# Performance work log

Measured on AMD Instinct MI355X. Metric: run time of the kernel, lower is better.

Reference implementation:

```python
import jax, jax.numpy as jnp
import numpy as np

DIM = 1536
NH = 12
HD = DIM // NH  # 128
F_, H_, W_ = 16, 16, 16
L = F_ * H_ * W_  # 4096


def _precompute_freqs(dim, max_positions, base=10000.0):
    # [max_positions, dim//2] angles
    half = dim // 2
    inv = 1.0 / base ** (np.arange(0, half * 2, 2, dtype=np.float32) / (half * 2))
    pos = np.arange(max_positions, dtype=np.float32)
    return pos[:, None] * inv[None, :]


def _get_3d_freqs(head_dim, F, H, W, base=10000.0):
    half_hd = head_dim // 2
    n_t = max(1, head_dim // 4 // 2)
    n_h = max(1, head_dim * 3 // 8 // 2)
    n_w = half_hd - n_t - n_h
    ft = _precompute_freqs(n_t * 2, F, base)  # [F, n_t]
    fh = _precompute_freqs(n_h * 2, H, base)  # [H, n_h]
    fw = _precompute_freqs(n_w * 2, W, base)  # [W, n_w]
    f_idx = np.broadcast_to(ft[:, None, None, :], (F, H, W, n_t))
    h_idx = np.broadcast_to(fh[None, :, None, :], (F, H, W, n_h))
    w_idx = np.broadcast_to(fw[None, None, :, :], (F, H, W, n_w))
    return np.concatenate([f_idx, h_idx, w_idx], axis=-1).reshape(F * H * W, half_hd)


def setup_inputs() -> dict:
    key = jax.random.key(0)
    ks = jax.random.split(key, 9)
    s = 1.0 / np.sqrt(DIM)
    x = jax.random.normal(ks[0], (1, L, DIM), dtype=jnp.float32)
    freqs = jnp.asarray(_get_3d_freqs(HD, F_, H_, W_), dtype=jnp.float32)
    Wq = jax.random.normal(ks[1], (DIM, DIM), dtype=jnp.float32) * s
    bq = jax.random.normal(ks[2], (DIM,), dtype=jnp.float32) * 0.01
    Wk = jax.random.normal(ks[3], (DIM, DIM), dtype=jnp.float32) * s
    bk = jax.random.normal(ks[4], (DIM,), dtype=jnp.float32) * 0.01
    Wv = jax.random.normal(ks[5], (DIM, DIM), dtype=jnp.float32) * s
    bv = jax.random.normal(ks[6], (DIM,), dtype=jnp.float32) * 0.01
    Wo = jax.random.normal(ks[7], (DIM, DIM), dtype=jnp.float32) * s
    bo = jax.random.normal(ks[8], (DIM,), dtype=jnp.float32) * 0.01
    return {"x": x, "freqs": freqs, "Wq": Wq, "bq": bq, "Wk": Wk, "bk": bk,
            "Wv": Wv, "bv": bv, "Wo": Wo, "bo": bo}


def _apply_rotary(t, cos_v, sin_v):
    # t: [B, Nh, L, Hd]; cos_v/sin_v: [L, Hd//2]
    B, Nh, Lq, Hd = t.shape
    t2 = t.reshape(B, Nh, Lq, Hd // 2, 2)
    x0, x1 = t2[..., 0], t2[..., 1]
    r0 = x0 * cos_v - x1 * sin_v
    r1 = x0 * sin_v + x1 * cos_v
    return jnp.stack([r0, r1], axis=-1).reshape(B, Nh, Lq, Hd)


def reference(x, freqs, Wq, bq, Wk, bk, Wv, bv, Wo, bo):
    B, Lq, D = x.shape
    Nh, Hd = NH, D // NH
    q = (x @ Wq + bq).reshape(B, Lq, Nh, Hd).transpose(0, 2, 1, 3)
    k = (x @ Wk + bk).reshape(B, Lq, Nh, Hd).transpose(0, 2, 1, 3)
    v = (x @ Wv + bv).reshape(B, Lq, Nh, Hd).transpose(0, 2, 1, 3)
    cos_v = jnp.cos(freqs)  # [L, Hd//2]
    sin_v = jnp.sin(freqs)
    q = _apply_rotary(q, cos_v, sin_v)
    k = _apply_rotary(k, cos_v, sin_v)
    scale = 1.0 / jnp.sqrt(jnp.asarray(Hd, dtype=x.dtype))
    scores = jnp.einsum('bhqd,bhkd->bhqk', q, k) * scale
    attn = jax.nn.softmax(scores, axis=-1)
    out = jnp.einsum('bhqk,bhkd->bhqd', attn, v)
    out = out.transpose(0, 2, 1, 3).reshape(B, Lq, D)
    return out @ Wo + bo
```

## Files before the change

### kernel.cpp

```cpp
#include <hip/hip_runtime.h>

#define DIM 1536
#define NH  12
#define HD  128
#define SEQ 4096

typedef unsigned short u16;
typedef unsigned int   u32;
typedef __attribute__((ext_vector_type(8))) short bf16x8;
typedef __attribute__((ext_vector_type(4))) float f32x4;

static __device__ __forceinline__ u16 f2bf(float f) {
    u32 u = __float_as_uint(f);
    u32 r = u + 0x7FFFu + ((u >> 16) & 1u);
    return (u16)(r >> 16);
}
static __device__ __forceinline__ float bf2f(u16 h) {
    return __uint_as_float(((u32)h) << 16);
}
static __device__ __forceinline__ u32 pack2(float a, float b) {
    return (u32)f2bf(a) | ((u32)f2bf(b) << 16);
}

#define GLL(g, s) __builtin_amdgcn_global_load_lds( \
    (const __attribute__((address_space(1))) void*)(g), \
    (__attribute__((address_space(3))) void*)(s), 16, 0, 0)

__global__ __launch_bounds__(256) void k_cvt_x(const float* __restrict__ x, u16* __restrict__ xb) {
    int gid = blockIdx.x * 256 + threadIdx.x;
    const float4* p = (const float4*)x + (size_t)gid * 2;
    float4 a = p[0], b = p[1];
    uint4 o;
    o.x = pack2(a.x, a.y); o.y = pack2(a.z, a.w);
    o.z = pack2(b.x, b.y); o.w = pack2(b.z, b.w);
    *(uint4*)(xb + (size_t)gid * 8) = o;
}

__global__ __launch_bounds__(256) void k_transpose_w(const float* __restrict__ Wq, const float* __restrict__ Wk,
                                                     const float* __restrict__ Wv, const float* __restrict__ Wo,
                                                     u16* __restrict__ wqkv, u16* __restrict__ wot) {
    __shared__ float tile[32][33];
    int z = blockIdx.z;
    const float* W = z == 0 ? Wq : z == 1 ? Wk : z == 2 ? Wv : Wo;
    u16* out = z < 3 ? (wqkv + (size_t)z * DIM * DIM) : wot;
    int tx = threadIdx.x, ty = threadIdx.y;
    int c0 = blockIdx.x * 32, r0 = blockIdx.y * 32;
#pragma unroll
    for (int i = 0; i < 4; i++)
        tile[ty + i * 8][tx] = W[(size_t)(r0 + ty + i * 8) * DIM + c0 + tx];
    __syncthreads();
#pragma unroll
    for (int i = 0; i < 4; i++)
        out[(size_t)(c0 + ty + i * 8) * DIM + r0 + tx] = f2bf(tile[tx][ty + i * 8]);
}

__global__ __launch_bounds__(256) void k_tr_v(const u16* __restrict__ vb, u16* __restrict__ vt) {
    __shared__ u16 tile[32][33];
    int h = blockIdx.z;
    int l0 = blockIdx.x * 32, d0 = blockIdx.y * 32;
    int tx = threadIdx.x, ty = threadIdx.y;
    const u16* src = vb + (size_t)h * SEQ * HD;
    u16* dst = vt + (size_t)h * HD * SEQ;
#pragma unroll
    for (int i = 0; i < 4; i++)
        tile[ty + i * 8][tx] = src[(size_t)(l0 + ty + i * 8) * HD + d0 + tx];
    __syncthreads();
#pragma unroll
    for (int i = 0; i < 4; i++)
        dst[(size_t)(d0 + ty + i * 8) * SEQ + l0 + tx] = tile[tx][ty + i * 8];
}

__global__ __launch_bounds__(256) void k_prep(const float* __restrict__ fr, const float* __restrict__ bq,
                                              const float* __restrict__ bk, const float* __restrict__ bv,
                                              float2* __restrict__ cs, float* __restrict__ bqkv) {
    int gid = blockIdx.x * 256 + threadIdx.x;
    float f = fr[gid];
    cs[gid] = make_float2(cosf(f), sinf(f));
    if (gid < 3 * DIM)
        bqkv[gid] = gid < DIM ? bq[gid] : gid < 2 * DIM ? bk[gid - DIM] : bv[gid - 2 * DIM];
}

__global__ __launch_bounds__(256) void k_gemm(const u16* __restrict__ A, const u16* __restrict__ B,
                                              const float* __restrict__ bias, int Kdim, int mode,
                                              u16* __restrict__ qo, u16* __restrict__ ko,
                                              u16* __restrict__ vo, float* __restrict__ outf) {
    __shared__ u16 As[128 * 32];
    __shared__ u16 Bs[128 * 32];
    const int tid = threadIdx.x;
    const int w = tid >> 6, l = tid & 63;
    const int wr = w >> 1, wc = w & 1;
    const int lr = l & 15, lg = l >> 4;
    const int m0 = blockIdx.y * 128, n0 = blockIdx.x * 128;
    f32x4 acc[4][4] = {};

    const int srow = l >> 2;
    const int scol = (((l & 3) * 16) ^ (((l >> 2) & 3) << 4)) >> 1;

    for (int kt = 0; kt < Kdim; kt += 32) {
        __syncthreads();
#pragma unroll
        for (int c2 = 0; c2 < 2; ++c2) {
            int c = w * 2 + c2;
            int row = c * 16 + srow;
            GLL(A + (size_t)(m0 + row) * Kdim + kt + scol, As + c * 512);
            GLL(B + (size_t)(n0 + row) * Kdim + kt + scol, Bs + c * 512);
        }
        __syncthreads();
        bf16x8 af[4], bg[4];
#pragma unroll
        for (int i = 0; i < 4; i++) {
            int co = (lg * 8) ^ ((lr & 3) << 3);
            af[i] = *(const bf16x8*)(As + (wr * 64 + i * 16 + lr) * 32 + co);
            bg[i] = *(const bf16x8*)(Bs + (wc * 64 + i * 16 + lr) * 32 + co);
        }
#pragma unroll
        for (int i = 0; i < 4; i++)
#pragma unroll
            for (int j = 0; j < 4; j++)
                acc[i][j] = __builtin_amdgcn_mfma_f32_16x16x32_bf16(af[i], bg[j], acc[i][j], 0, 0, 0);
    }

#pragma unroll
    for (int j = 0; j < 4; j++) {
        int gc = n0 + wc * 64 + j * 16 + lr;
        float bb = bias[gc];
#pragma unroll
        for (int i = 0; i < 4; i++) {
            int gr0 = m0 + wr * 64 + i * 16 + lg * 4;
            if (mode == 0) {
                int t = gc / DIM;
                int rr = gc % DIM;
                int hh = rr >> 7, hd = rr & 127;
                u16* dst = t == 0 ? qo : t == 1 ? ko : vo;
                size_t base = (size_t)hh * SEQ * HD + hd;
#pragma unroll
                for (int r = 0; r < 4; r++)
                    dst[base + (size_t)(gr0 + r) * HD] = f2bf(acc[i][j][r] + bb);
            } else {
#pragma unroll
                for (int r = 0; r < 4; r++)
                    outf[(size_t)(gr0 + r) * DIM + gc] = acc[i][j][r] + bb;
            }
        }
    }
}

__global__ __launch_bounds__(256) void k_rope(u16* __restrict__ qb, u16* __restrict__ kb,
                                              const float2* __restrict__ cs) {
    int gid = blockIdx.x * 256 + threadIdx.x;
    const int T = NH * SEQ * 64;
    u16* buf = gid < T ? qb : kb;
    int r = gid < T ? gid : gid - T;
    int hh = r / (SEQ * 64);
    int rr = r % (SEQ * 64);
    int ll = rr >> 6, ii = rr & 63;
    size_t off = ((size_t)hh * SEQ + ll) * HD + 2 * ii;
    u32 pk = *(const u32*)(buf + off);
    float x0 = bf2f((u16)(pk & 0xFFFFu)), x1 = bf2f((u16)(pk >> 16));
    float2 c = cs[ll * 64 + ii];
    float r0 = x0 * c.x - x1 * c.y;
    float r1 = x0 * c.y + x1 * c.x;
    *(u32*)(buf + off) = pack2(r0, r1);
}

__global__ __launch_bounds__(256, 3) void k_attn(const u16* __restrict__ qb, const u16* __restrict__ kbuf,
                                                 const u16* __restrict__ vt, u16* __restrict__ attnb) {
    __shared__ u16 Ks[64 * 128];
    __shared__ u16 Vs[128 * 64];
    __shared__ u32 Pl[4 * 16 * 36];
    const int tid = threadIdx.x;
    const int w = tid >> 6, l = tid & 63;
    const int lr = l & 15, lg = l >> 4;
    int bid = blockIdx.x;
    int gw = (bid & 7) * 96 + (bid >> 3);
    const int h = gw >> 6;
    const int q0 = (gw & 63) << 6;
    const size_t hb = (size_t)h * SEQ * HD;
    constexpr float SCL2 = 0.08838834764831845f * 1.4426950408889634f;
    constexpr float THR = 5.0f;

    bf16x8 qf[4];
    {
        int qrow = q0 + w * 16 + lr;
#pragma unroll
        for (int c = 0; c < 4; c++)
            qf[c] = *(const bf16x8*)(qb + hb + (size_t)qrow * HD + c * 32 + lg * 8);
    }
    f32x4 O[8] = {};
    float m_run = -1e30f, lsum = 0.f;
    u32* Plw = Pl + w * 576 + lr * 36;

    for (int kt = 0; kt < SEQ; kt += 64) {
        __syncthreads();
#pragma unroll
        for (int c = 0; c < 4; c++) {
            int cc = w * 4 + c;
            int key = cc * 4 + lg;
            int d0 = ((lr * 16) ^ ((key & 7) << 4)) >> 1;
            GLL(kbuf + hb + (size_t)(kt + key) * HD + d0, Ks + cc * 512);
            int dd = cc * 8 + (l >> 3);
            int c0 = (((l & 7) * 16) ^ ((l >> 3) << 4)) >> 1;
            GLL(vt + hb + (size_t)dd * SEQ + kt + c0, Vs + cc * 512);
        }
        __syncthreads();

        f32x4 ST[4];
#pragma unroll
        for (int jb = 0; jb < 4; jb++) {
            f32x4 st = {};
            int row = jb * 16 + lr;
            int rx = (row & 7) << 4;
#pragma unroll
            for (int c = 0; c < 4; c++) {
                int cb = ((c * 64 + lg * 16) ^ rx) >> 1;
                bf16x8 kf = *(const bf16x8*)(Ks + row * 128 + cb);
                st = __builtin_amdgcn_mfma_f32_16x16x32_bf16(kf, qf[c], st, 0, 0, 0);
            }
            ST[jb] = st;
        }

        float mx = ST[0][0];
#pragma unroll
        for (int jb = 0; jb < 4; jb++)
#pragma unroll
            for (int r = 0; r < 4; r++)
                mx = fmaxf(mx, ST[jb][r]);
        mx = fmaxf(mx, __shfl_xor(mx, 16));
        mx = fmaxf(mx, __shfl_xor(mx, 32));
        float mt = mx * SCL2;
        bool grow = mt > m_run + THR;
        float m_new = grow ? mt : m_run;
        if (__any(grow)) {
            float alpha = grow ? __builtin_amdgcn_exp2f(m_run - m_new) : 1.0f;
            lsum *= alpha;
            m_run = m_new;
            float aO[4];
#pragma unroll
            for (int r = 0; r < 4; r++)
                aO[r] = __shfl(alpha, lg * 4 + r);
#pragma unroll
            for (int f = 0; f < 8; f++)
#pragma unroll
                for (int r = 0; r < 4; r++)
                    O[f][r] *= aO[r];
        }
        float ps = 0.f;
#pragma unroll
        for (int jb = 0; jb < 4; jb++)
#pragma unroll
            for (int r = 0; r < 4; r++) {
                float p = __builtin_amdgcn_exp2f(fmaf(ST[jb][r], SCL2, -m_new));
                ST[jb][r] = p;
                ps += p;
            }
        lsum += ps;

#pragma unroll
        for (int jb = 0; jb < 4; jb++) {
            u32 p0, p1;
            asm("v_cvt_pk_bf16_f32 %0, %1, %2" : "=v"(p0) : "v"(ST[jb][0]), "v"(ST[jb][1]));
            asm("v_cvt_pk_bf16_f32 %0, %1, %2" : "=v"(p1) : "v"(ST[jb][2]), "v"(ST[jb][3]));
            Plw[jb * 8 + lg * 2 + 0] = p0;
            Plw[jb * 8 + lg * 2 + 1] = p1;
        }
        bf16x8 pa0 = *(const bf16x8*)(Plw + lg * 4);
        bf16x8 pa1 = *(const bf16x8*)(Plw + 16 + lg * 4);

#pragma unroll
        for (int f = 0; f < 8; f++) {
            int vrow = f * 16 + lr;
            int rx = (vrow & 7) << 4;
            bf16x8 v0 = *(const bf16x8*)(Vs + vrow * 64 + (((lg * 16) ^ rx) >> 1));
            O[f] = __builtin_amdgcn_mfma_f32_16x16x32_bf16(pa0, v0, O[f], 0, 0, 0);
            bf16x8 v1 = *(const bf16x8*)(Vs + vrow * 64 + (((64 + lg * 16) ^ rx) >> 1));
            O[f] = __builtin_amdgcn_mfma_f32_16x16x32_bf16(pa1, v1, O[f], 0, 0, 0);
        }
    }

    lsum += __shfl_xor(lsum, 16);
    lsum += __shfl_xor(lsum, 32);
    float li[4];
#pragma unroll
    for (int r = 0; r < 4; r++)
        li[r] = 1.0f / __shfl(lsum, lg * 4 + r);
#pragma unroll
    for (int f = 0; f < 8; f++) {
        int col = h * HD + f * 16 + lr;
#pragma unroll
        for (int r = 0; r < 4; r++) {
            int row = q0 + w * 16 + lg * 4 + r;
            attnb[(size_t)row * DIM + col] = f2bf(O[f][r] * li[r]);
        }
    }
}

extern "C" void kernel_launch(void* const* d_in, const int* in_sizes, int n_in,
                              void* d_out, int out_size, void* d_ws, size_t ws_size,
                              hipStream_t stream) {
    (void)in_sizes; (void)n_in; (void)out_size; (void)ws_size;
    const float* x  = (const float*)d_in[0];
    const float* fr = (const float*)d_in[1];
    const float* Wq = (const float*)d_in[2];
    const float* bq = (const float*)d_in[3];
    const float* Wk = (const float*)d_in[4];
    const float* bk = (const float*)d_in[5];
    const float* Wv = (const float*)d_in[6];
    const float* bv = (const float*)d_in[7];
    const float* Wo = (const float*)d_in[8];
    const float* bo = (const float*)d_in[9];
    float* out = (float*)d_out;

    char* ws = (char*)d_ws;
    size_t off = 0;
    auto alloc = [&](size_t b) { char* p = ws + off; off = (off + b + 255) & ~(size_t)255; return p; };
    u16*   xb    = (u16*)alloc((size_t)SEQ * DIM * 2);
    u16*   wqkv  = (u16*)alloc((size_t)3 * DIM * DIM * 2);
    u16*   wot   = (u16*)alloc((size_t)DIM * DIM * 2);
    float* bqkv  = (float*)alloc((size_t)3 * DIM * 4);
    u16*   qb    = (u16*)alloc((size_t)SEQ * DIM * 2);
    u16*   kb    = (u16*)alloc((size_t)SEQ * DIM * 2);
    u16*   vb    = (u16*)alloc((size_t)SEQ * DIM * 2);
    u16*   vtb   = (u16*)alloc((size_t)SEQ * DIM * 2);
    u16*   attnb = (u16*)alloc((size_t)SEQ * DIM * 2);
    float2* cs   = (float2*)alloc((size_t)SEQ * 64 * 8);

    k_cvt_x<<<3072, 256, 0, stream>>>(x, xb);
    k_transpose_w<<<dim3(48, 48, 4), dim3(32, 8), 0, stream>>>(Wq, Wk, Wv, Wo, wqkv, wot);
    k_prep<<<1024, 256, 0, stream>>>(fr, bq, bk, bv, cs, bqkv);
    k_gemm<<<dim3(36, 32), 256, 0, stream>>>(xb, wqkv, bqkv, DIM, 0, qb, kb, vb, nullptr);
    k_rope<<<24576, 256, 0, stream>>>(qb, kb, cs);
    k_tr_v<<<dim3(128, 4, 12), dim3(32, 8), 0, stream>>>(vb, vtb);
    k_attn<<<768, 256, 0, stream>>>(qb, kb, vtb, attnb);
    k_gemm<<<dim3(12, 32), 256, 0, stream>>>(attnb, wot, bo, DIM, 1, nullptr, nullptr, nullptr, out);
}
```

Before: 317.6 us.

## Double-buffer K/V tiles in attention and swizzle GEMM block order

The attention kernel now double-buffers the K and V shared-memory tiles. It issues the global-to-LDS loads for the next tile before computing on the current one, and waits on vmcnt instead of a full sync so memory latency overlaps with the MFMA work. It also raises wave priority around the MFMA sections and remaps GEMM block indices with an XCD-style swizzle to improve cache locality. Doubling the LDS buffers lowers the occupancy bound from 3 to 2 blocks per CU, which could offset the overlap benefit.

```diff
diff --git a/kernel.cpp b/kernel.cpp
--- a/kernel.cpp
+++ b/kernel.cpp
@@ -90,7 +90,10 @@
     const int w = tid >> 6, l = tid & 63;
     const int wr = w >> 1, wc = w & 1;
     const int lr = l & 15, lg = l >> 4;
-    const int m0 = blockIdx.y * 128, n0 = blockIdx.x * 128;
+    int nwg = gridDim.x * gridDim.y;
+    int bid = blockIdx.y * gridDim.x + blockIdx.x;
+    int swz = (bid & 7) * (nwg >> 3) + (bid >> 3);
+    const int m0 = (swz / gridDim.x) * 128, n0 = (swz % gridDim.x) * 128;
     f32x4 acc[4][4] = {};
 
     const int srow = l >> 2;
@@ -163,10 +166,10 @@
     *(u32*)(buf + off) = pack2(r0, r1);
 }
 
-__global__ __launch_bounds__(256, 3) void k_attn(const u16* __restrict__ qb, const u16* __restrict__ kbuf,
+__global__ __launch_bounds__(256, 2) void k_attn(const u16* __restrict__ qb, const u16* __restrict__ kbuf,
                                                  const u16* __restrict__ vt, u16* __restrict__ attnb) {
-    __shared__ u16 Ks[64 * 128];
-    __shared__ u16 Vs[128 * 64];
+    __shared__ u16 Ks[2][64 * 128];
+    __shared__ u16 Vs[2][128 * 64];
     __shared__ u32 Pl[4 * 16 * 36];
     const int tid = threadIdx.x;
     const int w = tid >> 6, l = tid & 63;
@@ -179,6 +182,9 @@
     constexpr float SCL2 = 0.08838834764831845f * 1.4426950408889634f;
     constexpr float THR = 5.0f;
 
+    const int vrow8 = l >> 3;
+    const int vc0 = (((l & 7) * 16) ^ (vrow8 << 4)) >> 1;
+
     bf16x8 qf[4];
     {
         int qrow = q0 + w * 16 + lr;
@@ -190,21 +196,38 @@
     float m_run = -1e30f, lsum = 0.f;
     u32* Plw = Pl + w * 576 + lr * 36;
 
-    for (int kt = 0; kt < SEQ; kt += 64) {
-        __syncthreads();
+    auto stage = [&](int buf, int kt) {
 #pragma unroll
         for (int c = 0; c < 4; c++) {
             int cc = w * 4 + c;
             int key = cc * 4 + lg;
-            int d0 = ((lr * 16) ^ ((key & 7) << 4)) >> 1;
-            GLL(kbuf + hb + (size_t)(kt + key) * HD + d0, Ks + cc * 512);
-            int dd = cc * 8 + (l >> 3);
-            int c0 = (((l & 7) * 16) ^ ((l >> 3) << 4)) >> 1;
-            GLL(vt + hb + (size_t)dd * SEQ + kt + c0, Vs + cc * 512);
-        }
-        __syncthreads();
+            int kd0 = ((lr * 16) ^ ((key & 7) << 4)) >> 1;
+            GLL(kbuf + hb + (size_t)(kt + key) * HD + kd0, Ks[buf] + cc * 512);
+            int dd = cc * 8 + vrow8;
+            GLL(vt + hb + (size_t)dd * SEQ + kt + vc0, Vs[buf] + cc * 512);
+        }
+    };
+
+    const int NT = SEQ / 64;
+    stage(0, 0);
+
+    for (int it = 0; it < NT; ++it) {
+        int cur = it & 1;
+        if (it + 1 < NT) {
+            stage(cur ^ 1, (it + 1) * 64);
+            asm volatile("s_waitcnt vmcnt(8)" ::: "memory");
+        } else {
+            asm volatile("s_waitcnt vmcnt(0)" ::: "memory");
+        }
+        __builtin_amdgcn_s_barrier();
+        asm volatile("" ::: "memory");
+        __builtin_amdgcn_sched_barrier(0);
+
+        const u16* Kc = Ks[cur];
+        const u16* Vc = Vs[cur];
 
         f32x4 ST[4];
+        __builtin_amdgcn_s_setprio(1);
 #pragma unroll
         for (int jb = 0; jb < 4; jb++) {
             f32x4 st = {};
@@ -213,11 +236,12 @@
 #pragma unroll
             for (int c = 0; c < 4; c++) {
                 int cb = ((c * 64 + lg * 16) ^ rx) >> 1;
-                bf16x8 kf = *(const bf16x8*)(Ks + row * 128 + cb);
+                bf16x8 kf = *(const bf16x8*)(Kc + row * 128 + cb);
                 st = __builtin_amdgcn_mfma_f32_16x16x32_bf16(kf, qf[c], st, 0, 0, 0);
             }
             ST[jb] = st;
         }
+        __builtin_amdgcn_s_setprio(0);
 
         float mx = ST[0][0];
 #pragma unroll
@@ -266,15 +290,21 @@
         bf16x8 pa0 = *(const bf16x8*)(Plw + lg * 4);
         bf16x8 pa1 = *(const bf16x8*)(Plw + 16 + lg * 4);
 
+        __builtin_amdgcn_s_setprio(1);
 #pragma unroll
         for (int f = 0; f < 8; f++) {
             int vrow = f * 16 + lr;
             int rx = (vrow & 7) << 4;
-            bf16x8 v0 = *(const bf16x8*)(Vs + vrow * 64 + (((lg * 16) ^ rx) >> 1));
+            bf16x8 v0 = *(const bf16x8*)(Vc + vrow * 64 + (((lg * 16) ^ rx) >> 1));
             O[f] = __builtin_amdgcn_mfma_f32_16x16x32_bf16(pa0, v0, O[f], 0, 0, 0);
-            bf16x8 v1 = *(const bf16x8*)(Vs + vrow * 64 + (((64 + lg * 16) ^ rx) >> 1));
+            bf16x8 v1 = *(const bf16x8*)(Vc + vrow * 64 + (((64 + lg * 16) ^ rx) >> 1));
             O[f] = __builtin_amdgcn_mfma_f32_16x16x32_bf16(pa1, v1, O[f], 0, 0, 0);
         }
+        __builtin_amdgcn_s_setprio(0);
+
+        asm volatile("" ::: "memory");
+        __builtin_amdgcn_s_barrier();
+        asm volatile("" ::: "memory");
     }
 
     lsum += __shfl_xor(lsum, 16);
```

After: 372.1 us. 1.17x slower.

## Rewrite attention with 32x32 MFMA, register-direct K/V loads and split-KV merge

Applied to the files above, without the earlier changes.

The attention kernel drops its LDS staging of K and V. Each wave now loads K and V fragments straight from global memory into registers and uses 32x32x16 bf16 MFMAs, passing P between lanes with permlane32 swaps instead of an LDS round trip. Within a block the key range is split between wave pairs, and the two partial softmax states are merged through shared memory at the end. Removing the per-tile syncthreads and LDS traffic costs redundant global loads per wave, and occupancy drops from 3 to 2 blocks. The GEMM also gets an XCD-aware block-index swizzle.

```diff
diff --git a/kernel.cpp b/kernel.cpp
--- a/kernel.cpp
+++ b/kernel.cpp
@@ -9,6 +9,7 @@
 typedef unsigned int   u32;
 typedef __attribute__((ext_vector_type(8))) short bf16x8;
 typedef __attribute__((ext_vector_type(4))) float f32x4;
+typedef __attribute__((ext_vector_type(16))) float f32x16;
 
 static __device__ __forceinline__ u16 f2bf(float f) {
     u32 u = __float_as_uint(f);
@@ -90,7 +91,10 @@
     const int w = tid >> 6, l = tid & 63;
     const int wr = w >> 1, wc = w & 1;
     const int lr = l & 15, lg = l >> 4;
-    const int m0 = blockIdx.y * 128, n0 = blockIdx.x * 128;
+    int nwg = gridDim.x * gridDim.y;
+    int bid = blockIdx.y * gridDim.x + blockIdx.x;
+    int swz = (bid & 7) * (nwg >> 3) + (bid >> 3);
+    const int m0 = (swz / gridDim.x) * 128, n0 = (swz % gridDim.x) * 128;
     f32x4 acc[4][4] = {};
 
     const int srow = l >> 2;
@@ -163,14 +167,13 @@
     *(u32*)(buf + off) = pack2(r0, r1);
 }
 
-__global__ __launch_bounds__(256, 3) void k_attn(const u16* __restrict__ qb, const u16* __restrict__ kbuf,
+__global__ __launch_bounds__(256, 2) void k_attn(const u16* __restrict__ qb, const u16* __restrict__ kbuf,
                                                  const u16* __restrict__ vt, u16* __restrict__ attnb) {
-    __shared__ u16 Ks[64 * 128];
-    __shared__ u16 Vs[128 * 64];
-    __shared__ u32 Pl[4 * 16 * 36];
+    __shared__ float MB[128][18];
     const int tid = threadIdx.x;
     const int w = tid >> 6, l = tid & 63;
-    const int lr = l & 15, lg = l >> 4;
+    const int qh = w & 1, kh = w >> 1;
+    const int g = l >> 5, qlane = l & 31;
     int bid = blockIdx.x;
     int gw = (bid & 7) * 96 + (bid >> 3);
     const int h = gw >> 6;
@@ -179,53 +182,33 @@
     constexpr float SCL2 = 0.08838834764831845f * 1.4426950408889634f;
     constexpr float THR = 5.0f;
 
-    bf16x8 qf[4];
+    bf16x8 qf[8];
     {
-        int qrow = q0 + w * 16 + lr;
-#pragma unroll
-        for (int c = 0; c < 4; c++)
-            qf[c] = *(const bf16x8*)(qb + hb + (size_t)qrow * HD + c * 32 + lg * 8);
-    }
-    f32x4 O[8] = {};
+        const u16* qp = qb + hb + (size_t)(q0 + qh * 32 + qlane) * HD + g * 8;
+#pragma unroll
+        for (int s = 0; s < 8; s++)
+            qf[s] = *(const bf16x8*)(qp + s * 16);
+    }
+    f32x16 O[4] = {};
     float m_run = -1e30f, lsum = 0.f;
-    u32* Plw = Pl + w * 576 + lr * 36;
+
+    const u16* kp = kbuf + hb + (size_t)(kh * 32 + qlane) * HD + g * 8;
+    const u16* vp = vt + hb + (size_t)qlane * SEQ + kh * 32 + g * 8;
 
     for (int kt = 0; kt < SEQ; kt += 64) {
-        __syncthreads();
-#pragma unroll
-        for (int c = 0; c < 4; c++) {
-            int cc = w * 4 + c;
-            int key = cc * 4 + lg;
-            int d0 = ((lr * 16) ^ ((key & 7) << 4)) >> 1;
-            GLL(kbuf + hb + (size_t)(kt + key) * HD + d0, Ks + cc * 512);
-            int dd = cc * 8 + (l >> 3);
-            int c0 = (((l & 7) * 16) ^ ((l >> 3) << 4)) >> 1;
-            GLL(vt + hb + (size_t)dd * SEQ + kt + c0, Vs + cc * 512);
-        }
-        __syncthreads();
-
-        f32x4 ST[4];
-#pragma unroll
-        for (int jb = 0; jb < 4; jb++) {
-            f32x4 st = {};
-            int row = jb * 16 + lr;
-            int rx = (row & 7) << 4;
-#pragma unroll
-            for (int c = 0; c < 4; c++) {
-                int cb = ((c * 64 + lg * 16) ^ rx) >> 1;
-                bf16x8 kf = *(const bf16x8*)(Ks + row * 128 + cb);
-                st = __builtin_amdgcn_mfma_f32_16x16x32_bf16(kf, qf[c], st, 0, 0, 0);
-            }
-            ST[jb] = st;
-        }
-
-        float mx = ST[0][0];
-#pragma unroll
-        for (int jb = 0; jb < 4; jb++)
-#pragma unroll
-            for (int r = 0; r < 4; r++)
-                mx = fmaxf(mx, ST[jb][r]);
-        mx = fmaxf(mx, __shfl_xor(mx, 16));
+        bf16x8 kf[8];
+        const u16* kpt = kp + (size_t)kt * HD;
+#pragma unroll
+        for (int s = 0; s < 8; s++)
+            kf[s] = *(const bf16x8*)(kpt + s * 16);
+        f32x16 ST = {};
+#pragma unroll
+        for (int s = 0; s < 8; s++)
+            ST = __builtin_amdgcn_mfma_f32_32x32x16_bf16(kf[s], qf[s], ST, 0, 0, 0);
+
+        float mx = ST[0];
+#pragma unroll
+        for (int r = 1; r < 16; r++) mx = fmaxf(mx, ST[r]);
         mx = fmaxf(mx, __shfl_xor(mx, 32));
         float mt = mx * SCL2;
         bool grow = mt > m_run + THR;
@@ -234,62 +217,76 @@
             float alpha = grow ? __builtin_amdgcn_exp2f(m_run - m_new) : 1.0f;
             lsum *= alpha;
             m_run = m_new;
-            float aO[4];
-#pragma unroll
-            for (int r = 0; r < 4; r++)
-                aO[r] = __shfl(alpha, lg * 4 + r);
-#pragma unroll
-            for (int f = 0; f < 8; f++)
-#pragma unroll
-                for (int r = 0; r < 4; r++)
-                    O[f][r] *= aO[r];
+#pragma unroll
+            for (int db = 0; db < 4; db++)
+#pragma unroll
+                for (int r = 0; r < 16; r++) O[db][r] *= alpha;
         }
         float ps = 0.f;
 #pragma unroll
-        for (int jb = 0; jb < 4; jb++)
-#pragma unroll
-            for (int r = 0; r < 4; r++) {
-                float p = __builtin_amdgcn_exp2f(fmaf(ST[jb][r], SCL2, -m_new));
-                ST[jb][r] = p;
-                ps += p;
+        for (int r = 0; r < 16; r++) {
+            float p = __builtin_amdgcn_exp2f(fmaf(ST[r], SCL2, -m_new));
+            ST[r] = p; ps += p;
+        }
+        lsum += ps;
+
+        u32 pw[2][4];
+#pragma unroll
+        for (int s2 = 0; s2 < 2; s2++) {
+            int rb = s2 * 8;
+            u32 a, b2, c2, d2;
+            asm("v_cvt_pk_bf16_f32 %0, %1, %2" : "=v"(a)  : "v"(ST[rb + 0]), "v"(ST[rb + 1]));
+            asm("v_cvt_pk_bf16_f32 %0, %1, %2" : "=v"(b2) : "v"(ST[rb + 2]), "v"(ST[rb + 3]));
+            asm("v_cvt_pk_bf16_f32 %0, %1, %2" : "=v"(c2) : "v"(ST[rb + 4]), "v"(ST[rb + 5]));
+            asm("v_cvt_pk_bf16_f32 %0, %1, %2" : "=v"(d2) : "v"(ST[rb + 6]), "v"(ST[rb + 7]));
+            asm("v_permlane32_swap_b32 %0, %1" : "+v"(a), "+v"(c2));
+            asm("v_permlane32_swap_b32 %0, %1" : "+v"(b2), "+v"(d2));
+            pw[s2][0] = a; pw[s2][1] = b2; pw[s2][2] = c2; pw[s2][3] = d2;
+        }
+
+        const u16* vpt = vp + kt;
+#pragma unroll
+        for (int s2 = 0; s2 < 2; s2++) {
+            union { u32 u[4]; bf16x8 v; } pf;
+            pf.u[0] = pw[s2][0]; pf.u[1] = pw[s2][1]; pf.u[2] = pw[s2][2]; pf.u[3] = pw[s2][3];
+#pragma unroll
+            for (int db = 0; db < 4; db++) {
+                bf16x8 vf = *(const bf16x8*)(vpt + (size_t)(db * 32) * SEQ + s2 * 16);
+                O[db] = __builtin_amdgcn_mfma_f32_32x32x16_bf16(vf, pf.v, O[db], 0, 0, 0);
             }
-        lsum += ps;
-
-#pragma unroll
-        for (int jb = 0; jb < 4; jb++) {
-            u32 p0, p1;
-            asm("v_cvt_pk_bf16_f32 %0, %1, %2" : "=v"(p0) : "v"(ST[jb][0]), "v"(ST[jb][1]));
-            asm("v_cvt_pk_bf16_f32 %0, %1, %2" : "=v"(p1) : "v"(ST[jb][2]), "v"(ST[jb][3]));
-            Plw[jb * 8 + lg * 2 + 0] = p0;
-            Plw[jb * 8 + lg * 2 + 1] = p1;
-        }
-        bf16x8 pa0 = *(const bf16x8*)(Plw + lg * 4);
-        bf16x8 pa1 = *(const bf16x8*)(Plw + 16 + lg * 4);
-
-#pragma unroll
-        for (int f = 0; f < 8; f++) {
-            int vrow = f * 16 + lr;
-            int rx = (vrow & 7) << 4;
-            bf16x8 v0 = *(const bf16x8*)(Vs + vrow * 64 + (((lg * 16) ^ rx) >> 1));
-            O[f] = __builtin_amdgcn_mfma_f32_16x16x32_bf16(pa0, v0, O[f], 0, 0, 0);
-            bf16x8 v1 = *(const bf16x8*)(Vs + vrow * 64 + (((64 + lg * 16) ^ rx) >> 1));
-            O[f] = __builtin_amdgcn_mfma_f32_16x16x32_bf16(pa1, v1, O[f], 0, 0, 0);
-        }
-    }
-
-    lsum += __shfl_xor(lsum, 16);
+        }
+    }
+
     lsum += __shfl_xor(lsum, 32);
-    float li[4];
-#pragma unroll
-    for (int r = 0; r < 4; r++)
-        li[r] = 1.0f / __shfl(lsum, lg * 4 + r);
-#pragma unroll
-    for (int f = 0; f < 8; f++) {
-        int col = h * HD + f * 16 + lr;
-#pragma unroll
-        for (int r = 0; r < 4; r++) {
-            int row = q0 + w * 16 + lg * 4 + r;
-            attnb[(size_t)row * DIM + col] = f2bf(O[f][r] * li[r]);
+
+    const int row = qh * 64 + l;
+    u16* op = attnb + (size_t)(q0 + qh * 32 + qlane) * DIM + h * HD;
+    __syncthreads();
+    if (kh == 1) { MB[row][16] = m_run; MB[row][17] = lsum; }
+    __syncthreads();
+    float a0 = 0.f, a1 = 0.f;
+    if (kh == 0) {
+        float m1 = MB[row][16], l1 = MB[row][17];
+        float mM = fmaxf(m_run, m1);
+        a0 = __builtin_amdgcn_exp2f(m_run - mM);
+        a1 = __builtin_amdgcn_exp2f(m1 - mM);
+        float linv = 1.0f / (lsum * a0 + l1 * a1);
+        a0 *= linv; a1 *= linv;
+    }
+#pragma unroll
+    for (int db = 0; db < 4; db++) {
+        __syncthreads();
+        if (kh == 1) {
+#pragma unroll
+            for (int r = 0; r < 16; r++) MB[row][r] = O[db][r];
+        }
+        __syncthreads();
+        if (kh == 0) {
+#pragma unroll
+            for (int r = 0; r < 16; r++) {
+                int d = db * 32 + (r & 3) + 8 * (r >> 2) + 4 * g;
+                op[d] = f2bf(O[db][r] * a0 + MB[row][r] * a1);
+            }
         }
     }
 }
```

Result: slower. 516.2 us (+62.5%).
